# Kernel optimization log

Measured on AMD Instinct MI355X. Metric: run time of the kernel, lower is better.

The kernel has to match this reference:

```python
import jax, jax.numpy as jnp
import numpy as np

N = 16384      # nodes
E = 131072     # edges
D = 768        # in_size = hid_size = out_size (LayerNorm(768) hardcoded)
NT = 4         # num edge types (TypedLinear num_types)
NB = 3         # num bases (basis regularizer)
LN_EPS = 1e-5


def _layernorm(x, gamma, beta):
    mu = jnp.mean(x, axis=-1, keepdims=True)
    var = jnp.mean(jnp.square(x - mu), axis=-1, keepdims=True)
    return (x - mu) * jax.lax.rsqrt(var + LN_EPS) * gamma + beta


def setup_inputs() -> dict:
    key = jax.random.key(0)
    ks = jax.random.split(key, 16)
    s = 0.02  # weight init scale
    return {
        "h": jax.random.normal(ks[0], (N, D), jnp.float32),
        # TypedLinear basis params: W = sum_b coeff[t,b] * basis[b]
        "W_text": jax.random.normal(ks[1], (NB, D, D), jnp.float32) * s,
        "coeff_text": jax.random.normal(ks[2], (NT, NB), jnp.float32),
        "W_user": jax.random.normal(ks[3], (NB, D, D), jnp.float32) * s,
        "coeff_user": jax.random.normal(ks[4], (NT, NB), jnp.float32),
        "W_dst": jax.random.normal(ks[5], (NB, D, D), jnp.float32) * s,
        "coeff_dst": jax.random.normal(ks[6], (NT, NB), jnp.float32),
        "ln_gamma": jnp.ones((D,), jnp.float32),
        "ln_beta": jnp.zeros((D,), jnp.float32),
        "W_lin": jax.random.normal(ks[7], (2 * D, D), jnp.float32) * s,
        "b_lin": jnp.zeros((D,), jnp.float32),
        "src": jax.random.randint(ks[8], (E,), 0, N, dtype=jnp.int32),
        "dst": jax.random.randint(ks[9], (E,), 0, N, dtype=jnp.int32),
        "etype": jax.random.randint(ks[10], (E,), 0, NT, dtype=jnp.int32),
        "hete": jax.random.randint(ks[11], (E,), 0, 2, dtype=jnp.int32),
    }


def reference(h, W_text, coeff_text, W_user, coeff_user, W_dst, coeff_dst,
              ln_gamma, ln_beta, W_lin, b_lin, src, dst, etype, hete):
    # eval mode: dropout = identity
    x = _layernorm(h, ln_gamma, ln_beta)                       # [N, D]
    # Typed-linear via basis decomposition, folded per (type, node): [NT, N, D]
    Ht = jnp.einsum('nd,bdh,tb->tnh', x, W_text, coeff_text)
    Hu = jnp.einsum('nd,bdh,tb->tnh', x, W_user, coeff_user)
    Hd = jnp.einsum('nd,bdh,tb->tnh', x, W_dst, coeff_dst)

    mask = hete > 0                                            # hete vs homo edges
    # per-edge routed source message: [E, D]
    ef = jnp.where(mask[:, None],
                   jax.nn.relu(Ht[etype, src]),
                   jax.nn.relu(Hu[etype, src]))
    # Original concatenates [hete_feat, homo_feat] along edge dim, i.e. a stable
    # permutation putting hete edges first; dst features stay in original order.
    perm = jnp.argsort((~mask).astype(jnp.int32), stable=True)
    feat_perm = ef[perm]                                       # [E, D]
    dfeat = jax.nn.relu(Hd[etype, dst])                        # [E, D]
    m = jnp.concatenate([feat_perm, dfeat], axis=-1)           # [E, 2D]
    # scatter-sum messages to destination nodes
    n = jax.ops.segment_sum(m, dst, num_segments=N)            # [N, 2D]
    z = jax.nn.relu(n @ W_lin + b_lin)                         # [N, D]
    zn = jnp.linalg.norm(z, ord=2, axis=1, keepdims=True)
    zn = jnp.where(zn == 0, jnp.asarray(1.0, z.dtype), zn)
    return z / zn
```

## Files before the change

kernel.cpp:

```cpp
#include <hip/hip_runtime.h>
#include <hip/hip_bf16.h>
#include <cstdint>

static constexpr int N_  = 16384;
static constexpr int E_  = 131072;
static constexpr int D_  = 768;
static constexpr int D2_ = 1536;
static constexpr int DSQ_ = D_ * D_;

static constexpr size_t OFF_XB   = 0;
static constexpr size_t OFF_WCT  = 25165824;
static constexpr size_t OFF_WLT  = 39321600;
static constexpr size_t OFF_NB16 = 41680896;
static constexpr size_t OFF_H4   = 92012544;
static constexpr size_t OFF_ZB   = 92012544;
static constexpr size_t OFF_N1C  = 192675840;
static constexpr size_t OFF_TG   = 217841664;
static constexpr size_t OFF_PAY  = 218365952;
static constexpr size_t OFF_CNT  = 218890240;
static constexpr size_t OFF_BASE = 219152384;
static constexpr size_t OFF_CUR  = 219217936;
static constexpr size_t OFF_BC   = 219283472;
static constexpr size_t OFF_SCAN = 219285520;

typedef __attribute__((ext_vector_type(8))) short short8v;
typedef __attribute__((ext_vector_type(4))) float floatx4;

__device__ __forceinline__ void gld16(const void* g, void* l) {
  __builtin_amdgcn_global_load_lds(
      (const __attribute__((address_space(1))) unsigned int*)g,
      (__attribute__((address_space(3))) unsigned int*)l, 16, 0, 0);
}

__device__ __forceinline__ float b2f(short u) {
  union { unsigned int i; float f; } x;
  x.i = ((unsigned int)(unsigned short)u) << 16;
  return x.f;
}

__device__ __forceinline__ float wave_sum(float v) {
#pragma unroll
  for (int o = 32; o; o >>= 1) v += __shfl_down(v, o, 64);
  return v;
}

__global__ __launch_bounds__(256) void combine_wt_kernel(
    const float* __restrict__ Wt, const float* __restrict__ ct,
    const float* __restrict__ Wu, const float* __restrict__ cu,
    const float* __restrict__ Wd, const float* __restrict__ cd,
    __hip_bfloat16* __restrict__ WcT) {
  int i  = blockIdx.x * 256 + threadIdx.x;
  int ft = blockIdx.y;
  int f = ft >> 2, t = ft & 3;
  const float* W = (f == 0) ? Wt : ((f == 1) ? Wu : Wd);
  const float* c = ((f == 0) ? ct : ((f == 1) ? cu : cd)) + t * 3;
  float v = c[0] * W[i] + c[1] * W[DSQ_ + i] + c[2] * W[2 * DSQ_ + i];
  int d = i / D_, h = i % D_;
  WcT[(size_t)ft * DSQ_ + (size_t)h * D_ + d] = __float2bfloat16(v);
}

__global__ __launch_bounds__(256) void wlint_kernel(
    const float* __restrict__ W, __hip_bfloat16* __restrict__ WT) {
  int i = blockIdx.x * 256 + threadIdx.x;
  int k = i / D_, h = i % D_;
  WT[(size_t)h * D2_ + k] = __float2bfloat16(W[i]);
}

__global__ __launch_bounds__(256) void ln_kernel(
    const float* __restrict__ h, const float* __restrict__ gamma,
    const float* __restrict__ beta, __hip_bfloat16* __restrict__ x) {
  int v = blockIdx.x, tid = threadIdx.x;
  const float* hr = h + (size_t)v * D_;
  float e0 = hr[tid], e1 = hr[tid + 256], e2 = hr[tid + 512];
  float s = e0 + e1 + e2;
  float q = e0 * e0 + e1 * e1 + e2 * e2;
  __shared__ float red[8];
  __shared__ float mv[2];
  float ws_ = wave_sum(s), wq = wave_sum(q);
  int lane = tid & 63, w = tid >> 6;
  if (lane == 0) { red[w] = ws_; red[4 + w] = wq; }
  __syncthreads();
  if (tid == 0) {
    float S = red[0] + red[1] + red[2] + red[3];
    float Q = red[4] + red[5] + red[6] + red[7];
    float mu = S * (1.0f / D_);
    float var = Q * (1.0f / D_) - mu * mu;
    mv[0] = mu;
    mv[1] = rsqrtf(var + 1e-5f);
  }
  __syncthreads();
  float mu = mv[0], rstd = mv[1];
  __hip_bfloat16* xr = x + (size_t)v * D_;
  xr[tid]       = __float2bfloat16((e0 - mu) * rstd * gamma[tid]       + beta[tid]);
  xr[tid + 256] = __float2bfloat16((e1 - mu) * rstd * gamma[tid + 256] + beta[tid + 256]);
  xr[tid + 512] = __float2bfloat16((e2 - mu) * rstd * gamma[tid + 512] + beta[tid + 512]);
}

__global__ __launch_bounds__(256) void edge_a_kernel(
    const int* __restrict__ hete, const int* __restrict__ dst,
    const int* __restrict__ etype, int* __restrict__ blockcnt,
    int* __restrict__ cnt4) {
  int j = blockIdx.x * 256 + threadIdx.x;
  int flag = hete[j] > 0;
  unsigned long long m = __ballot(flag);
  __shared__ int wsum[4];
  int lane = threadIdx.x & 63, w = threadIdx.x >> 6;
  if (lane == 0) wsum[w] = __popcll(m);
  __syncthreads();
  if (threadIdx.x == 0)
    blockcnt[blockIdx.x] = wsum[0] + wsum[1] + wsum[2] + wsum[3];
  atomicAdd(&cnt4[dst[j] * 4 + etype[j]], 1);
}

__global__ __launch_bounds__(512) void scan_kernel(
    const int* __restrict__ blockcnt, int* __restrict__ scanout) {
  __shared__ int s[512];
  int t = threadIdx.x;
  int v = blockcnt[t];
  s[t] = v;
  __syncthreads();
  for (int o = 1; o < 512; o <<= 1) {
    int add = (t >= o) ? s[t - o] : 0;
    __syncthreads();
    s[t] += add;
    __syncthreads();
  }
  scanout[t] = s[t] - v;
  if (t == 511) scanout[512] = s[511];
}

__global__ __launch_bounds__(256) void edge_b_kernel(
    const int* __restrict__ hete, const int* __restrict__ dst,
    const int* __restrict__ scanout, int* __restrict__ target) {
  int j = blockIdx.x * 256 + threadIdx.x;
  int flag = hete[j] > 0;
  unsigned long long m = __ballot(flag);
  __shared__ int wsum[4];
  int lane = threadIdx.x & 63, w = threadIdx.x >> 6;
  if (lane == 0) wsum[w] = __popcll(m);
  __syncthreads();
  int wpre = 0;
#pragma unroll
  for (int i = 0; i < 4; i++) wpre += (i < w) ? wsum[i] : 0;
  int lpre = __popcll(m & ((1ull << lane) - 1ull));
  int hcum = scanout[blockIdx.x] + wpre + lpre;
  int K = scanout[512];
  int e = flag ? hcum : (K + j - hcum);
  target[j] = dst[e];
}

__global__ __launch_bounds__(1024) void base_scan_kernel(
    const int* __restrict__ cnt4, int* __restrict__ base) {
  __shared__ int s[1024];
  int t = threadIdx.x;
  int loc[16];
  int sum = 0;
#pragma unroll
  for (int i = 0; i < 16; i++) {
    int v = t * 16 + i;
    int d = cnt4[v * 4] + cnt4[v * 4 + 1] + cnt4[v * 4 + 2] + cnt4[v * 4 + 3];
    loc[i] = sum;
    sum += d;
  }
  s[t] = sum;
  __syncthreads();
  for (int o = 1; o < 1024; o <<= 1) {
    int add = (t >= o) ? s[t - o] : 0;
    __syncthreads();
    s[t] += add;
    __syncthreads();
  }
  int pre = t ? s[t - 1] : 0;
#pragma unroll
  for (int i = 0; i < 16; i++) base[t * 16 + i] = pre + loc[i];
  if (t == 1023) base[N_] = s[1023];
}

__global__ __launch_bounds__(256) void edge_sort_kernel(
    const int* __restrict__ target, const int* __restrict__ src,
    const int* __restrict__ etype, const int* __restrict__ hete,
    const int* __restrict__ base, int* __restrict__ cursor,
    int* __restrict__ payload) {
  int j = blockIdx.x * 256 + threadIdx.x;
  int v = target[j];
  int p = base[v] + atomicAdd(&cursor[v], 1);
  int g = ((hete[j] > 0) ? 0 : 4) + etype[j];
  payload[p] = (g << 14) | src[j];
}

template <bool FIRST>
__global__ __launch_bounds__(256) void gather_n1_kernel(
    const __hip_bfloat16* __restrict__ H, const int* __restrict__ base,
    const int* __restrict__ payload, __hip_bfloat16* __restrict__ n1c,
    __hip_bfloat16* __restrict__ nb16, int g0) {
  int wv = threadIdx.x >> 6, lane = threadIdx.x & 63;
  int v = blockIdx.x * 4 + wv;
  int b0 = base[v], b1 = base[v + 1];
  float acc[12];
  if (FIRST) {
#pragma unroll
    for (int i = 0; i < 12; i++) acc[i] = 0.f;
  } else {
    short8v a8 = *(const short8v*)(n1c + (size_t)v * D_ + lane * 8);
    short4  b4 = *(const short4*)(n1c + (size_t)v * D_ + 512 + lane * 4);
#pragma unroll
    for (int i = 0; i < 8; i++) acc[i] = b2f(a8[i]);
    acc[8] = b2f(b4.x); acc[9] = b2f(b4.y);
    acc[10] = b2f(b4.z); acc[11] = b2f(b4.w);
  }
  for (int idx = b0; idx < b1; ++idx) {
    int pl = payload[idx];
    int g = (pl >> 14) - g0;
    if ((unsigned)g > 3u) continue;
    const __hip_bfloat16* row = H + ((size_t)g * N_ + (pl & 16383)) * D_;
    short8v a8 = *(const short8v*)(row + lane * 8);
    short4  b4 = *(const short4*)(row + 512 + lane * 4);
#pragma unroll
    for (int i = 0; i < 8; i++) acc[i] += b2f(a8[i]);
    acc[8] += b2f(b4.x); acc[9] += b2f(b4.y);
    acc[10] += b2f(b4.z); acc[11] += b2f(b4.w);
  }
  __hip_bfloat16 o[12];
#pragma unroll
  for (int i = 0; i < 12; i++) o[i] = __float2bfloat16(acc[i]);
  if (FIRST) {
    *(short8v*)(n1c + (size_t)v * D_ + lane * 8) = *(const short8v*)o;
    *(short4*)(n1c + (size_t)v * D_ + 512 + lane * 4) = *(const short4*)(o + 8);
  } else {
    *(short8v*)(nb16 + (size_t)v * D2_ + lane * 8) = *(const short8v*)o;
    *(short4*)(nb16 + (size_t)v * D2_ + 512 + lane * 4) = *(const short4*)(o + 8);
  }
}

__global__ __launch_bounds__(256) void combine_n2_kernel(
    const __hip_bfloat16* __restrict__ H4, const int* __restrict__ cnt4,
    __hip_bfloat16* __restrict__ nb16) {
  size_t i = ((size_t)blockIdx.x * 256 + threadIdx.x) * 8;
  int v = (int)(i / D_);
  int k = (int)(i % D_);
  float acc[8] = {0.f, 0.f, 0.f, 0.f, 0.f, 0.f, 0.f, 0.f};
#pragma unroll
  for (int t = 0; t < 4; t++) {
    float c = (float)cnt4[v * 4 + t];
    if (c != 0.f) {
      short8v hv = *(const short8v*)(H4 + (size_t)t * N_ * D_ + i);
#pragma unroll
      for (int j = 0; j < 8; j++) acc[j] += c * b2f(hv[j]);
    }
  }
  __hip_bfloat16 o[8];
#pragma unroll
  for (int j = 0; j < 8; j++) o[j] = __float2bfloat16(acc[j]);
  *(short8v*)(nb16 + (size_t)v * D2_ + D_ + k) = *(const short8v*)o;
}

__device__ __forceinline__ int fragaddr(int r, int p) {
  int u = r >> 1;
  int s = ((r & 1) << 2) | p;
  return u * 128 + ((s ^ (u & 7)) << 4);
}

__device__ __forceinline__ void stage_kh(const __hip_bfloat16* X, int K,
                                         int rowbase, int kglob, char* unit,
                                         int tid) {
#pragma unroll
  for (int j = 0; j < 2; j++) {
    int q = j * 512 + tid;
    int u = q >> 3;
    int sp = q & 7;
    int s = sp ^ (u & 7);
    int r = (u << 1) | (s >> 2);
    int p = s & 3;
    gld16(X + (size_t)(rowbase + r) * K + kglob + p * 8, unit + q * 16);
  }
}

template <bool BIAS, bool OUTBF16>
__global__ __launch_bounds__(512, 1) void gemm8p_kernel(
    const __hip_bfloat16* __restrict__ A, const __hip_bfloat16* __restrict__ BT0,
    const float* __restrict__ bias, void* __restrict__ Cv,
    int M, int N, int K, size_t strideB, size_t strideC) {
  __shared__ char lds[131072];
  const int tid = threadIdx.x, lane = tid & 63, wv = tid >> 6;
  const int wr = wv >> 2, wcn = wv & 3;
  int gx = gridDim.x, gz = gridDim.z;
  int nwg = gx * gridDim.y * gz;
  int id = (blockIdx.z * gridDim.y + blockIdx.y) * gx + blockIdx.x;
  int s = (id & 7) * (nwg >> 3) + (id >> 3);
  int bx = s % gx;
  int rem = s / gx;
  int z = rem % gz;
  int by = rem / gz;
  const __hip_bfloat16* BT = BT0 + (size_t)z * strideB;
  int row0 = by * 256, col0 = bx * 256;
  const int nt = K >> 6, ni = nt >> 1;

  floatx4 acc[8][4];
#pragma unroll
  for (int i = 0; i < 8; i++)
#pragma unroll
    for (int j = 0; j < 4; j++) acc[i][j] = floatx4{0.f, 0.f, 0.f, 0.f};

  stage_kh(A, K, row0, 0, lds, tid);
  stage_kh(BT, K, col0, 0, lds + 32768, tid);
  stage_kh(A, K, row0, 32, lds + 16384, tid);
  stage_kh(BT, K, col0, 32, lds + 49152, tid);
  asm volatile("s_waitcnt vmcnt(4)" ::: "memory");
  __builtin_amdgcn_s_barrier();
  asm volatile("" ::: "memory");

  for (int it = 0; it < ni; ++it) {
#pragma unroll
    for (int half = 0; half < 2; ++half) {
      char* rbuf = lds + (half << 16);
      char* sbuf = lds + ((half ^ 1) << 16);
      int stile = 2 * it + 1 + half;
      bool do_stage = stile < nt;
      int kg0 = stile * 64;
      short8v af[8];
#pragma unroll
      for (int ks = 0; ks < 2; ++ks) {
#pragma unroll
        for (int ch = 0; ch < 2; ++ch) {
          char* Au = rbuf + ks * 16384;
          char* Bu = rbuf + 32768 + ks * 16384;
          if (ch == 0) {
#pragma unroll
            for (int rf = 0; rf < 8; ++rf) {
              int r = wr * 128 + rf * 16 + (lane & 15);
              af[rf] = *(const short8v*)(Au + fragaddr(r, lane >> 4));
            }
          }
          short8v bfr[2];
#pragma unroll
          for (int nf = 0; nf < 2; ++nf) {
            int r = wcn * 64 + ch * 32 + nf * 16 + (lane & 15);
            bfr[nf] = *(const short8v*)(Bu + fragaddr(r, lane >> 4));
          }
          if (do_stage) {
            if (ch == 0)
              stage_kh(A, K, row0, kg0 + ks * 32, sbuf + ks * 16384, tid);
            else
              stage_kh(BT, K, col0, kg0 + ks * 32, sbuf + 32768 + ks * 16384,
                       tid);
          }
          asm volatile("" ::: "memory");
          __builtin_amdgcn_s_barrier();
          asm volatile("" ::: "memory");
          __builtin_amdgcn_s_setprio(1);
#pragma unroll
          for (int rf = 0; rf < 8; ++rf)
#pragma unroll
            for (int nf = 0; nf < 2; ++nf)
              acc[rf][ch * 2 + nf] = __builtin_amdgcn_mfma_f32_16x16x32_bf16(
                  af[rf], bfr[nf], acc[rf][ch * 2 + nf], 0, 0, 0);
          __builtin_amdgcn_s_setprio(0);
          if (ch == 1) {
            if (it == ni - 1 && half == 1) {
              if (ks == 0) asm volatile("s_waitcnt vmcnt(0)" ::: "memory");
            } else {
              asm volatile("s_waitcnt vmcnt(4)" ::: "memory");
            }
          }
          asm volatile("" ::: "memory");
          __builtin_amdgcn_s_barrier();
          asm volatile("" ::: "memory");
        }
      }
    }
  }
#pragma unroll
  for (int rf = 0; rf < 8; ++rf) {
#pragma unroll
    for (int j = 0; j < 4; ++j) {
      int col = col0 + wcn * 64 + (j >> 1) * 32 + (j & 1) * 16 + (lane & 15);
      float bv = BIAS ? bias[col] : 0.f;
#pragma unroll
      for (int q = 0; q < 4; ++q) {
        int row = row0 + wr * 128 + rf * 16 + (lane >> 4) * 4 + q;
        float v = fmaxf(acc[rf][j][q] + bv, 0.f);
        if constexpr (OUTBF16) {
          ((__hip_bfloat16*)Cv + (size_t)z * strideC)[(size_t)row * N + col] =
              __float2bfloat16(v);
        } else {
          ((float*)Cv + (size_t)z * strideC)[(size_t)row * N + col] = v;
        }
      }
    }
  }
}

__global__ __launch_bounds__(256) void norm_kernel(
    const float* __restrict__ z, float* __restrict__ out) {
  int v = blockIdx.x, tid = threadIdx.x;
  const float* zr = z + (size_t)v * D_;
  float e0 = zr[tid], e1 = zr[tid + 256], e2 = zr[tid + 512];
  float q = e0 * e0 + e1 * e1 + e2 * e2;
  __shared__ float red[4];
  __shared__ float sc;
  float wq = wave_sum(q);
  int lane = tid & 63, w = tid >> 6;
  if (lane == 0) red[w] = wq;
  __syncthreads();
  if (tid == 0) {
    float S = red[0] + red[1] + red[2] + red[3];
    float norm = sqrtf(S);
    sc = (norm == 0.f) ? 1.f : (1.f / norm);
  }
  __syncthreads();
  float s = sc;
  float* orow = out + (size_t)v * D_;
  orow[tid]       = e0 * s;
  orow[tid + 256] = e1 * s;
  orow[tid + 512] = e2 * s;
}

extern "C" void kernel_launch(void* const* d_in, const int* in_sizes, int n_in,
                              void* d_out, int out_size, void* d_ws,
                              size_t ws_size, hipStream_t stream) {
  (void)in_sizes; (void)n_in; (void)out_size; (void)ws_size;
  const float* h      = (const float*)d_in[0];
  const float* W_text = (const float*)d_in[1];
  const float* c_text = (const float*)d_in[2];
  const float* W_user = (const float*)d_in[3];
  const float* c_user = (const float*)d_in[4];
  const float* W_dst  = (const float*)d_in[5];
  const float* c_dst  = (const float*)d_in[6];
  const float* gamma  = (const float*)d_in[7];
  const float* beta   = (const float*)d_in[8];
  const float* W_lin  = (const float*)d_in[9];
  const float* b_lin  = (const float*)d_in[10];
  const int* src      = (const int*)d_in[11];
  const int* dst      = (const int*)d_in[12];
  const int* etype    = (const int*)d_in[13];
  const int* hete     = (const int*)d_in[14];
  float* out          = (float*)d_out;

  char* ws = (char*)d_ws;
  __hip_bfloat16* xb   = (__hip_bfloat16*)(ws + OFF_XB);
  __hip_bfloat16* WcT  = (__hip_bfloat16*)(ws + OFF_WCT);
  __hip_bfloat16* WlT  = (__hip_bfloat16*)(ws + OFF_WLT);
  __hip_bfloat16* nb16 = (__hip_bfloat16*)(ws + OFF_NB16);
  __hip_bfloat16* H4   = (__hip_bfloat16*)(ws + OFF_H4);
  float* zbuf          = (float*)(ws + OFF_ZB);
  __hip_bfloat16* n1c  = (__hip_bfloat16*)(ws + OFF_N1C);
  int* target   = (int*)(ws + OFF_TG);
  int* payload  = (int*)(ws + OFF_PAY);
  int* cnt4     = (int*)(ws + OFF_CNT);
  int* base     = (int*)(ws + OFF_BASE);
  int* cursor   = (int*)(ws + OFF_CUR);
  int* blockcnt = (int*)(ws + OFF_BC);
  int* scanout  = (int*)(ws + OFF_SCAN);

  hipMemsetAsync(cnt4, 0, (size_t)N_ * 4 * 4, stream);
  hipMemsetAsync(cursor, 0, (size_t)N_ * 4, stream);

  combine_wt_kernel<<<dim3(DSQ_ / 256, 12), 256, 0, stream>>>(
      W_text, c_text, W_user, c_user, W_dst, c_dst, WcT);
  wlint_kernel<<<(D2_ * D_) / 256, 256, 0, stream>>>(W_lin, WlT);
  ln_kernel<<<N_, 256, 0, stream>>>(h, gamma, beta, xb);
  edge_a_kernel<<<E_ / 256, 256, 0, stream>>>(hete, dst, etype, blockcnt, cnt4);
  scan_kernel<<<1, 512, 0, stream>>>(blockcnt, scanout);
  edge_b_kernel<<<E_ / 256, 256, 0, stream>>>(hete, dst, scanout, target);
  base_scan_kernel<<<1, 1024, 0, stream>>>(cnt4, base);
  edge_sort_kernel<<<E_ / 256, 256, 0, stream>>>(target, src, etype, hete,
                                                 base, cursor, payload);

  const size_t HSTRIDE = (size_t)N_ * D_;
  const dim3 ggrid(D_ / 256, N_ / 256, 4);

  gemm8p_kernel<false, true><<<ggrid, 512, 0, stream>>>(
      xb, WcT + (size_t)8 * DSQ_, nullptr, H4, N_, D_, D_, DSQ_, HSTRIDE);
  combine_n2_kernel<<<(N_ * D_) / (256 * 8), 256, 0, stream>>>(H4, cnt4, nb16);

  gemm8p_kernel<false, true><<<ggrid, 512, 0, stream>>>(
      xb, WcT, nullptr, H4, N_, D_, D_, DSQ_, HSTRIDE);
  gather_n1_kernel<true><<<N_ / 4, 256, 0, stream>>>(H4, base, payload, n1c,
                                                     nb16, 0);
  gemm8p_kernel<false, true><<<ggrid, 512, 0, stream>>>(
      xb, WcT + (size_t)4 * DSQ_, nullptr, H4, N_, D_, D_, DSQ_, HSTRIDE);
  gather_n1_kernel<false><<<N_ / 4, 256, 0, stream>>>(H4, base, payload, n1c,
                                                      nb16, 4);

  gemm8p_kernel<true, false><<<dim3(D_ / 256, N_ / 256, 1), 512, 0, stream>>>(
      nb16, WlT, b_lin, zbuf, N_, D_, D2_, 0, 0);
  norm_kernel<<<N_, 256, 0, stream>>>(zbuf, out);
}
```

Measured before the change: 494.7 us.

## Deepen GEMM LDS pipeline to a nine-slot ring buffer with more loads in flight

Replaces the two-stage double-buffered LDS pipeline in the bf16 MFMA GEMM with a 9-unit rotating ring of 16 KB slots, prefetching up to two k-tiles ahead. Waits are relaxed to vmcnt(8) so more global loads stay outstanding while the MFMAs run. LDS grows from 128 KB to 144 KB per block, which fits one workgroup per CU but makes the vmcnt accounting and slot indexing harder to get right.

```diff
diff --git a/kernel.cpp b/kernel.cpp
--- a/kernel.cpp
+++ b/kernel.cpp
@@ -275,12 +275,14 @@
   }
 }
 
+__device__ __forceinline__ int wrap9(int x) { return x >= 9 ? x - 9 : x; }
+
 template <bool BIAS, bool OUTBF16>
 __global__ __launch_bounds__(512, 1) void gemm8p_kernel(
     const __hip_bfloat16* __restrict__ A, const __hip_bfloat16* __restrict__ BT0,
     const float* __restrict__ bias, void* __restrict__ Cv,
     int M, int N, int K, size_t strideB, size_t strideC) {
-  __shared__ char lds[131072];
+  __shared__ char lds[147456];
   const int tid = threadIdx.x, lane = tid & 63, wv = tid >> 6;
   const int wr = wv >> 2, wcn = wv & 3;
   int gx = gridDim.x, gz = gridDim.z;
@@ -293,7 +295,7 @@
   int by = rem / gz;
   const __hip_bfloat16* BT = BT0 + (size_t)z * strideB;
   int row0 = by * 256, col0 = bx * 256;
-  const int nt = K >> 6, ni = nt >> 1;
+  const int nt = K >> 6;
 
   floatx4 acc[8][4];
 #pragma unroll
@@ -302,72 +304,80 @@
     for (int j = 0; j < 4; j++) acc[i][j] = floatx4{0.f, 0.f, 0.f, 0.f};
 
   stage_kh(A, K, row0, 0, lds, tid);
-  stage_kh(BT, K, col0, 0, lds + 32768, tid);
-  stage_kh(A, K, row0, 32, lds + 16384, tid);
-  stage_kh(BT, K, col0, 32, lds + 49152, tid);
-  asm volatile("s_waitcnt vmcnt(4)" ::: "memory");
+  stage_kh(BT, K, col0, 0, lds + 16384, tid);
+  stage_kh(A, K, row0, 32, lds + 2 * 16384, tid);
+  stage_kh(BT, K, col0, 32, lds + 3 * 16384, tid);
+  stage_kh(A, K, row0, 64, lds + 4 * 16384, tid);
+  stage_kh(BT, K, col0, 64, lds + 5 * 16384, tid);
+  asm volatile("s_waitcnt vmcnt(8)" ::: "memory");
   __builtin_amdgcn_s_barrier();
   asm volatile("" ::: "memory");
 
-  for (int it = 0; it < ni; ++it) {
-#pragma unroll
-    for (int half = 0; half < 2; ++half) {
-      char* rbuf = lds + (half << 16);
-      char* sbuf = lds + ((half ^ 1) << 16);
-      int stile = 2 * it + 1 + half;
-      bool do_stage = stile < nt;
-      int kg0 = stile * 64;
-      short8v af[8];
-#pragma unroll
-      for (int ks = 0; ks < 2; ++ks) {
-#pragma unroll
-        for (int ch = 0; ch < 2; ++ch) {
-          char* Au = rbuf + ks * 16384;
-          char* Bu = rbuf + 32768 + ks * 16384;
-          if (ch == 0) {
-#pragma unroll
-            for (int rf = 0; rf < 8; ++rf) {
-              int r = wr * 128 + rf * 16 + (lane & 15);
-              af[rf] = *(const short8v*)(Au + fragaddr(r, lane >> 4));
-            }
-          }
-          short8v bfr[2];
-#pragma unroll
-          for (int nf = 0; nf < 2; ++nf) {
-            int r = wcn * 64 + ch * 32 + nf * 16 + (lane & 15);
-            bfr[nf] = *(const short8v*)(Bu + fragaddr(r, lane >> 4));
-          }
-          if (do_stage) {
-            if (ch == 0)
-              stage_kh(A, K, row0, kg0 + ks * 32, sbuf + ks * 16384, tid);
-            else
-              stage_kh(BT, K, col0, kg0 + ks * 32, sbuf + 32768 + ks * 16384,
-                       tid);
-          }
-          asm volatile("" ::: "memory");
-          __builtin_amdgcn_s_barrier();
-          asm volatile("" ::: "memory");
-          __builtin_amdgcn_s_setprio(1);
-#pragma unroll
-          for (int rf = 0; rf < 8; ++rf)
-#pragma unroll
-            for (int nf = 0; nf < 2; ++nf)
-              acc[rf][ch * 2 + nf] = __builtin_amdgcn_mfma_f32_16x16x32_bf16(
-                  af[rf], bfr[nf], acc[rf][ch * 2 + nf], 0, 0, 0);
-          __builtin_amdgcn_s_setprio(0);
-          if (ch == 1) {
-            if (it == ni - 1 && half == 1) {
-              if (ks == 0) asm volatile("s_waitcnt vmcnt(0)" ::: "memory");
-            } else {
-              asm volatile("s_waitcnt vmcnt(4)" ::: "memory");
-            }
-          }
-          asm volatile("" ::: "memory");
-          __builtin_amdgcn_s_barrier();
-          asm volatile("" ::: "memory");
+  int su = 0;
+  for (int t = 0; t < nt; ++t) {
+    char* A0u = lds + su * 16384;
+    char* B0u = lds + wrap9(su + 1) * 16384;
+    char* A1u = lds + wrap9(su + 2) * 16384;
+    char* B1u = lds + wrap9(su + 3) * 16384;
+    char* st6 = lds + wrap9(su + 6) * 16384;
+    char* st7 = lds + wrap9(su + 7) * 16384;
+    char* st8 = lds + wrap9(su + 8) * 16384;
+    char* st9 = lds + su * 16384;
+    short8v af[8];
+#pragma unroll
+    for (int j = 0; j < 4; ++j) {
+      const int ks = j >> 1, ch = j & 1;
+      char* Au = (ks == 0) ? A0u : A1u;
+      char* Bu = (ks == 0) ? B0u : B1u;
+      if (ch == 0) {
+#pragma unroll
+        for (int rf = 0; rf < 8; ++rf) {
+          int r = wr * 128 + rf * 16 + (lane & 15);
+          af[rf] = *(const short8v*)(Au + fragaddr(r, lane >> 4));
         }
       }
+      short8v bfr[2];
+#pragma unroll
+      for (int nf = 0; nf < 2; ++nf) {
+        int r = wcn * 64 + ch * 32 + nf * 16 + (lane & 15);
+        bfr[nf] = *(const short8v*)(Bu + fragaddr(r, lane >> 4));
+      }
+      if (j == 0 && t + 1 < nt)
+        stage_kh(A, K, row0, (t + 1) * 64 + 32, st6, tid);
+      if (j == 1 && t + 1 < nt)
+        stage_kh(BT, K, col0, (t + 1) * 64 + 32, st7, tid);
+      if (j == 2 && t + 2 < nt)
+        stage_kh(A, K, row0, (t + 2) * 64, st8, tid);
+      if (j == 3 && t + 2 < nt)
+        stage_kh(BT, K, col0, (t + 2) * 64, st9, tid);
+      asm volatile("" ::: "memory");
+      __builtin_amdgcn_s_barrier();
+      asm volatile("" ::: "memory");
+      __builtin_amdgcn_s_setprio(1);
+#pragma unroll
+      for (int rf = 0; rf < 8; ++rf)
+#pragma unroll
+        for (int nf = 0; nf < 2; ++nf)
+          acc[rf][ch * 2 + nf] = __builtin_amdgcn_mfma_f32_16x16x32_bf16(
+              af[rf], bfr[nf], acc[rf][ch * 2 + nf], 0, 0, 0);
+      __builtin_amdgcn_s_setprio(0);
+      if (j == 0) {
+        if (t < nt - 1) asm volatile("s_waitcnt vmcnt(8)" ::: "memory");
+        else            asm volatile("s_waitcnt vmcnt(4)" ::: "memory");
+      } else if (j == 1) {
+        if (t < nt - 1) asm volatile("s_waitcnt vmcnt(8)" ::: "memory");
+        else            asm volatile("s_waitcnt vmcnt(0)" ::: "memory");
+      } else if (j == 2) {
+        if (t < nt - 1) asm volatile("s_waitcnt vmcnt(8)" ::: "memory");
+      } else {
+        if (t < nt - 2)      asm volatile("s_waitcnt vmcnt(8)" ::: "memory");
+        else if (t == nt - 2) asm volatile("s_waitcnt vmcnt(4)" ::: "memory");
+      }
+      asm volatile("" ::: "memory");
+      __builtin_amdgcn_s_barrier();
+      asm volatile("" ::: "memory");
     }
+    su = wrap9(su + 4);
   }
 #pragma unroll
   for (int rf = 0; rf < 8; ++rf) {
```

New measurement: 501.6 us. About the same (+1.4%).
